# Performance work log

Hardware: AMD Instinct MI355X
Metric: run time of the kernel (lower is better)

## Reference

```python
import jax, jax.numpy as jnp
import numpy as np

VSN = 1e-12  # VERY_SMALL_NUMBER
B, N, IN_DIM = 48, 512, 400
ENC, HID, OUT, NREL = 256, 128, 128, 53
NUM_PERS, KNN, EPS, SKIP = 4, 10, 0.3, 0.8


def setup_inputs() -> dict:
    key = jax.random.key(0)
    ks = jax.random.split(key, 12)
    context = jax.random.normal(ks[0], (B, N, IN_DIM), dtype=jnp.float32)
    context_lens = jax.random.randint(ks[1], (B,), N // 2, N + 1)
    s1 = jax.random.randint(ks[2], (B,), 0, N - 16)
    e1 = s1 + jax.random.randint(ks[3], (B,), 1, 8)
    s2 = jax.random.randint(ks[4], (B,), 0, N - 16)
    e2 = s2 + jax.random.randint(ks[5], (B,), 1, 8)
    mentions = jnp.stack([s1, e1, s2, e2], axis=-1)  # [B,4]
    sc = lambda d: 1.0 / np.sqrt(d)
    w_enc = jax.random.normal(ks[6], (IN_DIM, ENC), dtype=jnp.float32) * sc(IN_DIM)
    b_enc = jnp.zeros((ENC,), jnp.float32)
    gl_weight = jax.random.normal(ks[7], (NUM_PERS, IN_DIM), dtype=jnp.float32)
    gcn_w1 = jax.random.normal(ks[8], (ENC, HID), dtype=jnp.float32) * sc(ENC)
    gcn_b1 = jnp.zeros((HID,), jnp.float32)
    gcn_w2 = jax.random.normal(ks[9], (HID, OUT), dtype=jnp.float32) * sc(HID)
    gcn_b2 = jnp.zeros((OUT,), jnp.float32)
    lin_w = jax.random.normal(ks[10], (OUT, NREL), dtype=jnp.float32) * sc(OUT)
    lin_b = jnp.zeros((NREL,), jnp.float32)
    return dict(context=context, context_lens=context_lens, mentions=mentions,
                w_enc=w_enc, b_enc=b_enc, gl_weight=gl_weight,
                gcn_w1=gcn_w1, gcn_b1=gcn_b1, gcn_w2=gcn_w2, gcn_b2=gcn_b2,
                lin_w=lin_w, lin_b=lin_b)


def _knn_init_adj(feats, mask):
    # binarized kNN graph on raw features + symmetric normalization
    mask2d = mask[:, :, None] * mask[:, None, :]
    att = jnp.einsum('bnd,bmd->bnm', feats, feats) * mask2d
    _, idx = jax.lax.top_k(att, KNN)                      # [B,N,K]
    adj = jnp.zeros((B, N, N), feats.dtype).at[
        jnp.arange(B)[:, None, None], jnp.arange(N)[None, :, None], idx].set(1.0)
    adj = adj * mask2d
    rowsum = jnp.clip(adj.sum(-1), VSN, None)
    rinv = (rowsum ** -0.5) * mask                        # [B,N]
    return rinv[:, :, None] * adj * rinv[:, None, :]


def _weighted_cosine(feats, gl_weight, mask):
    # multi-perspective weighted cosine similarity, epsilon-sparsified (>=0 adj)
    ctx = feats[None] * gl_weight[:, None, None, :]       # [P,B,N,D]
    ctx = ctx / jnp.clip(jnp.linalg.norm(ctx, axis=-1, keepdims=True), VSN, None)
    att = jnp.einsum('pbnd,pbmd->pbnm', ctx, ctx).mean(0)  # [B,N,N]
    mask2d = mask[:, :, None] * mask[:, None, :]
    att = att * mask2d                                    # markoff_value = 0
    return att * (att > EPS).astype(att.dtype)


def _merge(enc_seq, start, end):
    w_ids = jnp.arange(N)[None, :]                        # [1,N]
    ind = ((w_ids >= start[:, None]) & (w_ids <= end[:, None])).astype(enc_seq.dtype)
    return jnp.einsum('bn,bnd->bd', ind, enc_seq) / ind.sum(-1, keepdims=True)


def reference(context, context_lens, mentions, w_enc, b_enc, gl_weight,
              gcn_w1, gcn_b1, gcn_w2, gcn_b2, lin_w, lin_b):
    mask = (jnp.arange(N)[None, :] < context_lens[:, None]).astype(jnp.float32)
    # init kNN adjacency on detached raw features
    init_adj = _knn_init_adj(jax.lax.stop_gradient(context), mask)
    # context encoder (linear projection stand-in for the LSTM ctx_encoder)
    enc = context @ w_enc + b_enc                          # [B,N,ENC]
    # learned graph: row-normalize then skip-connect with init_adj
    raw_adj = _weighted_cosine(context, gl_weight, mask)
    adj = raw_adj / jnp.clip(raw_adj.sum(-1, keepdims=True), VSN, None)
    adj = SKIP * init_adj + (1.0 - SKIP) * adj
    # 2-hop GCN encoder
    h = jax.nn.relu(jnp.einsum('bnm,bmd->bnd', adj, enc) @ gcn_w1 + gcn_b1)
    node_vec = jnp.einsum('bnm,bmd->bnd', adj, h) @ gcn_w2 + gcn_b2  # [B,N,OUT]
    # graph maxpool over nodes + mention merging (broadcast-mask averaging)
    pooled = node_vec.max(axis=1)                          # [B,OUT]
    arg1 = _merge(node_vec, mentions[:, 0], mentions[:, 1])
    arg2 = _merge(node_vec, mentions[:, 2], mentions[:, 3])
    return (pooled + arg1 + arg2) @ lin_w + lin_b          # [B,NREL]
```

## Files before the change

kernel.cpp:

```cpp
#include <hip/hip_runtime.h>
#include <math.h>

constexpr int cB = 48, cN = 512, cIN = 400;
constexpr int cENC = 256, cHID = 128, cOUT = 128, cNREL = 53;
constexpr int cKNN = 10;
constexpr float cVSN = 1e-12f;
constexpr float cEPS = 0.3f;

constexpr int KP = 416;
constexpr size_t ARRSZ = (size_t)cB * cN * KP;
constexpr int NBN = cB * cN;
constexpr size_t NADJ = (size_t)cB * cN * cN;
constexpr size_t NE1 = (size_t)NBN * 128;

typedef _Float16 f16;
typedef _Float16 f16x8 __attribute__((ext_vector_type(8)));
typedef float f32x4 __attribute__((ext_vector_type(4)));

__device__ inline void gload16(const void* g, void* l) {
    __builtin_amdgcn_global_load_lds(
        (const __attribute__((address_space(1))) unsigned int*)g,
        (__attribute__((address_space(3))) unsigned int*)l, 16, 0, 0);
}

#define MFMA16(a, b, c) __builtin_amdgcn_mfma_f32_16x16x32_f16((a), (b), (c), 0, 0, 0)

__global__ __launch_bounds__(256) void k_prep0(
    const float* __restrict__ X,
    const float* __restrict__ w_enc, const float* __restrict__ w1,
    const float* __restrict__ b_enc, const float* __restrict__ w2,
    f16* __restrict__ XH, f16* __restrict__ XL,
    f16* __restrict__ wc1H, float* __restrict__ bc1p, f16* __restrict__ w2tH)
{
    int bid = blockIdx.x;
    int t = threadIdx.x;
    if (bid <= KP) {
        int d = bid;
        __shared__ float wred[2][128];
        int o = t & 127, half = t >> 7;
        if (d < cIN) {
            float acc = 0.f;
            const float* we = w_enc + (size_t)d * cENC + half * 128;
            const float* w1p = w1 + (size_t)half * 128 * cHID + o;
            #pragma unroll 8
            for (int e = 0; e < 128; ++e) acc += we[e] * w1p[(size_t)e * cHID];
            wred[half][o] = acc;
            __syncthreads();
            if (half == 0) wc1H[(size_t)o * KP + d] = (f16)(wred[0][o] + wred[1][o]);
        } else if (d < KP) {
            if (t < 128) wc1H[(size_t)o * KP + d] = (f16)0.f;
        } else {
            float acc = 0.f;
            const float* w1p = w1 + (size_t)half * 128 * cHID + o;
            #pragma unroll 8
            for (int e = 0; e < 128; ++e) acc += b_enc[half * 128 + e] * w1p[(size_t)e * cHID];
            wred[half][o] = acc;
            __syncthreads();
            if (half == 0) bc1p[o] = wred[0][o] + wred[1][o];
        }
        if (d < cHID && t < 128) w2tH[(size_t)t * cHID + d] = (f16)w2[(size_t)d * cOUT + t];
        return;
    }
    int row = (bid - (KP + 1)) * 4 + (t >> 6);
    int k8 = t & 63;
    if (k8 >= 52) return;
    size_t obase = (size_t)row * KP + k8 * 8;
    if (k8 < 50) {
        const float* x = X + (size_t)row * cIN + k8 * 8;
        float4 xa = *(const float4*)x;
        float4 xb = *(const float4*)(x + 4);
        float xv[8] = {xa.x, xa.y, xa.z, xa.w, xb.x, xb.y, xb.z, xb.w};
        f16x8 vh, vl;
        #pragma unroll
        for (int e = 0; e < 8; ++e) {
            f16 hh = (f16)xv[e];
            vh[e] = hh;
            vl[e] = (f16)(xv[e] - (float)hh);
        }
        *(f16x8*)(XH + obase) = vh;
        *(f16x8*)(XL + obase) = vl;
    } else {
        f16x8 z = (f16x8)(f16)0.f;
        *(f16x8*)(XH + obase) = z;
        *(f16x8*)(XL + obase) = z;
    }
}

__global__ __launch_bounds__(256) void k_norms(const float* __restrict__ X,
                                               const int* __restrict__ lens,
                                               const float* __restrict__ glw,
                                               float* __restrict__ maskA,
                                               float* __restrict__ invnM)
{
    int row = blockIdx.x;
    int t = threadIdx.x;
    int w = t >> 6, lane = t & 63;
    __shared__ float sw[4];
    int b = row >> 9, n = row & (cN - 1);
    float s = 0.f;
    if (lane < 50) {
        int k = lane * 8;
        const float* x = X + (size_t)row * cIN + k;
        const float* g = glw + (size_t)w * cIN + k;
        float4 xa = *(const float4*)x, xb = *(const float4*)(x + 4);
        float4 ga = *(const float4*)g, gb = *(const float4*)(g + 4);
        float xv[8] = {xa.x, xa.y, xa.z, xa.w, xb.x, xb.y, xb.z, xb.w};
        float gv[8] = {ga.x, ga.y, ga.z, ga.w, gb.x, gb.y, gb.z, gb.w};
        #pragma unroll
        for (int e = 0; e < 8; ++e) {
            float tt = xv[e] * gv[e];
            s += tt * tt;
        }
    }
    #pragma unroll
    for (int off = 32; off; off >>= 1) s += __shfl_xor(s, off, 64);
    if (lane == 0) sw[w] = s;
    __syncthreads();
    if (t == 0) {
        float m = (n < lens[b]) ? 1.0f : 0.0f;
        float4 iv;
        iv.x = m / fmaxf(sqrtf(sw[0]), cVSN);
        iv.y = m / fmaxf(sqrtf(sw[1]), cVSN);
        iv.z = m / fmaxf(sqrtf(sw[2]), cVSN);
        iv.w = m / fmaxf(sqrtf(sw[3]), cVSN);
        *(float4*)&invnM[(size_t)row * 4] = iv;
        maskA[row] = m;
    }
}

__global__ __launch_bounds__(256, 3) void k_sim_mfma(
    const f16* __restrict__ XH, const f16* __restrict__ XL,
    const float* __restrict__ glw, const int* __restrict__ lens,
    const float* __restrict__ maskA, const float* __restrict__ invnM,
    float* __restrict__ G0, f16* __restrict__ RAh)
{
    int L = blockIdx.x + (blockIdx.y << 3) + (blockIdx.z << 6);
    int xcd = L & 7, j0 = L >> 3;
    int work = xcd * 384 + j0;
    const int b = work >> 6;
    int rem = work & 63;
    const int n0 = (rem >> 3) * 64, m0 = (rem & 7) * 64;

    const int t = threadIdx.x;
    const int w = t >> 6, lane = t & 63;
    const int wr = w >> 1, wc = w & 1;
    const int lr = lane & 15, lc = lane >> 4;

    const size_t rowBaseB = (size_t)b * cN;
    const int len = lens[b];

    if (n0 >= len || m0 >= len) return;

    __shared__ f16 lds[3][8192];
    __shared__ f16 w2l[4][KP];

    for (int i = t; i < 4 * KP; i += 256) {
        int p = i / KP, d = i - p * KP;
        float g = (d < cIN) ? glw[p * cIN + d] : 0.f;
        w2l[p][d] = (f16)(g * g);
    }

    f32x4 accG[2][2], accP[4][2][2];
    #pragma unroll
    for (int i = 0; i < 2; ++i)
        #pragma unroll
        for (int jj = 0; jj < 2; ++jj) {
            accG[i][jj] = (f32x4)0.f;
            #pragma unroll
            for (int p = 0; p < 4; ++p) accP[p][i][jj] = (f32x4)0.f;
        }

    constexpr int NPAN = KP / 32;

#define SIM_STAGE(buf, pan) do { \
    const int kk0_ = (pan) * 32; \
    _Pragma("unroll") \
    for (int q = 0; q < 4; ++q) { \
        int c_ = w + q * 4;                \
        int tt_ = c_ >> 2, rq_ = c_ & 3; \
        int row_ = rq_ * 16 + (lane >> 2); \
        int kcg_ = (lane & 3) ^ (row_ & 3) ^ ((row_ >> 2) & 3); \
        const f16* arr_ = (tt_ & 1) ? XL : XH; \
        int rb_ = (tt_ < 2) ? n0 : m0; \
        const f16* g_ = arr_ + (rowBaseB + rb_ + row_) * (size_t)KP + kk0_ + kcg_ * 8; \
        gload16(g_, (void*)&lds[buf][tt_ * 2048 + rq_ * 512]); \
    } \
} while (0)

    SIM_STAGE(0, 0);
    SIM_STAGE(1, 1);
    __syncthreads();

    for (int pan = 0; pan < NPAN; ++pan) {
        int cur = pan % 3;
        if (pan + 2 < NPAN) SIM_STAGE((pan + 2) % 3, pan + 2);
        const f16x8* L8 = (const f16x8*)lds[cur];
        const int kk0 = pan * 32;
        f16x8 aH[2], aL[2], bH[2], bL[2], wp[4];
        #pragma unroll
        for (int i = 0; i < 2; ++i) {
            int r = wr * 32 + i * 16 + lr;
            int cell = r * 4 + (lc ^ (r & 3) ^ ((r >> 2) & 3));
            aH[i] = L8[cell];
            aL[i] = L8[256 + cell];
        }
        #pragma unroll
        for (int jj = 0; jj < 2; ++jj) {
            int r = wc * 32 + jj * 16 + lr;
            int cell = r * 4 + (lc ^ (r & 3) ^ ((r >> 2) & 3));
            bH[jj] = L8[512 + cell];
            bL[jj] = L8[768 + cell];
        }
        #pragma unroll
        for (int p = 0; p < 4; ++p) wp[p] = *(const f16x8*)&w2l[p][kk0 + lc * 8];

        __builtin_amdgcn_s_setprio(1);
        #pragma unroll
        for (int i = 0; i < 2; ++i)
            #pragma unroll
            for (int jj = 0; jj < 2; ++jj) {
                accG[i][jj] = MFMA16(aH[i], bH[jj], accG[i][jj]);
                accG[i][jj] = MFMA16(aH[i], bL[jj], accG[i][jj]);
                accG[i][jj] = MFMA16(aL[i], bH[jj], accG[i][jj]);
            }
        #pragma unroll
        for (int p = 0; p < 4; ++p)
            #pragma unroll
            for (int i = 0; i < 2; ++i) {
                f16x8 ap = aH[i] * wp[p];
                #pragma unroll
                for (int jj = 0; jj < 2; ++jj)
                    accP[p][i][jj] = MFMA16(ap, bH[jj], accP[p][i][jj]);
            }
        __builtin_amdgcn_s_setprio(0);

        if (pan < NPAN - 1) {
            if (pan + 2 < NPAN) {
                asm volatile("s_waitcnt vmcnt(4)" ::: "memory");
            } else {
                asm volatile("s_waitcnt vmcnt(0)" ::: "memory");
            }
            asm volatile("s_waitcnt lgkmcnt(0)" ::: "memory");
            __builtin_amdgcn_s_barrier();
        }
    }
#undef SIM_STAGE

    #pragma unroll
    for (int i = 0; i < 2; ++i) {
        #pragma unroll
        for (int jj = 0; jj < 2; ++jj) {
            int m = m0 + wc * 32 + jj * 16 + lr;
            size_t rowm = rowBaseB + m;
            float mskm = maskA[rowm];
            float4 im = *(const float4*)&invnM[rowm * 4];
            #pragma unroll
            for (int v = 0; v < 4; ++v) {
                int n = n0 + wr * 32 + i * 16 + lc * 4 + v;
                size_t rown = rowBaseB + n;
                float4 in_ = *(const float4*)&invnM[rown * 4];
                float g = accG[i][jj][v] * maskA[rown] * mskm;
                float s = 0.25f * (accP[0][i][jj][v] * in_.x * im.x
                                 + accP[1][i][jj][v] * in_.y * im.y
                                 + accP[2][i][jj][v] * in_.z * im.z
                                 + accP[3][i][jj][v] * in_.w * im.w);
                float rv = (s > cEPS) ? s : 0.f;
                __builtin_nontemporal_store(g, &G0[rown * cN + m]);
                RAh[rown * cN + m] = (f16)rv;
            }
        }
    }
}

__global__ void k_topk(const float* __restrict__ G0, const float* __restrict__ mask,
                       const int* __restrict__ lens,
                       int* __restrict__ kidx, float* __restrict__ rinv)
{
    int row = blockIdx.x * 4 + (threadIdx.x >> 6);
    int lane = threadIdx.x & 63;
    int b = row >> 9, n = row & (cN - 1);
    int len = lens[b];
    if (n >= len) {
        if (lane < cKNN) kidx[row * cKNN + lane] = lane;
        if (lane == 0) rinv[row] = 0.f;
        return;
    }
    int lenc = (len + 63) & ~63;
    const float* g = G0 + (long long)row * cN;
    float val[8];
    #pragma unroll
    for (int k = 0; k < 8; ++k) {
        int col = lane + 64 * k;
        val[k] = (col < lenc) ? __builtin_nontemporal_load(&g[col]) : -INFINITY;
    }
    float cnt = 0.f;
    long long mbase = (long long)b * cN;
    for (int r = 0; r < cKNN; ++r) {
        float best = val[0];
        #pragma unroll
        for (int k = 1; k < 8; ++k) best = fmaxf(best, val[k]);
        #pragma unroll
        for (int off = 32; off; off >>= 1) best = fmaxf(best, __shfl_xor(best, off, 64));
        int sl = -1;
        #pragma unroll
        for (int k = 7; k >= 0; --k) if (val[k] == best) sl = k;
        unsigned long long holders = __ballot(sl >= 0);
        int src = (int)(__ffsll((long long)holders) - 1);
        int mycol = lane + (sl << 6);
        int col = __shfl(mycol, src, 64);
        if (lane == src) val[sl] = -INFINITY;
        if (lane == 0) {
            kidx[row * cKNN + r] = col;
            cnt += mask[mbase + col];
        }
    }
    if (lane == 0) rinv[row] = rsqrtf(fmaxf(cnt, cVSN));
}

__global__ void k_adj2(const f16* __restrict__ RAh, const float* __restrict__ rinv,
                       const int* __restrict__ kidx, const int* __restrict__ lens,
                       f16* __restrict__ adjH, float* __restrict__ adjrs)
{
    int row = blockIdx.x;
    int t = threadIdx.x;
    int b = row >> 9, n = row & (cN - 1);
    int len = lens[b];
    long long base = (long long)row * cN;
    if (n >= len) {
        adjH[base + t] = (f16)0.f;
        adjH[base + t + 256] = (f16)0.f;
        if (t == 0) adjrs[row] = 0.f;
        return;
    }
    int w = t >> 6, lane = t & 63;
    __shared__ int sidx[cKNN];
    __shared__ float srv[cKNN];
    __shared__ float red[4];
    long long bbase = (long long)(row & ~(cN - 1));
    if (t < cKNN) {
        int c = kidx[row * cKNN + t];
        sidx[t] = c;
        srv[t] = rinv[bbase + c];
    }
    float ra0 = (t < len) ? (float)RAh[base + t] : 0.f;
    float ra1 = (t + 256 < len) ? (float)RAh[base + t + 256] : 0.f;
    float s = ra0 + ra1;
    #pragma unroll
    for (int off = 32; off; off >>= 1) s += __shfl_xor(s, off, 64);
    if (lane == 0) red[w] = s;
    __syncthreads();
    float rsum = red[0] + red[1] + red[2] + red[3];
    float inv_rs = 1.0f / fmaxf(rsum, cVSN);
    float rn = rinv[row];
    float osum = 0.f;
    #pragma unroll
    for (int mi = 0; mi < 2; ++mi) {
        int m = t + mi * 256;
        float ra = mi ? ra1 : ra0;
        float v = 0.2f * ra * inv_rs;
        #pragma unroll
        for (int k = 0; k < cKNN; ++k)
            if (m == sidx[k]) v += 0.8f * rn * srv[k];
        adjH[base + m] = (f16)v;
        osum += v;
    }
    #pragma unroll
    for (int off = 32; off; off >>= 1) osum += __shfl_xor(osum, off, 64);
    __syncthreads();
    if (lane == 0) red[w] = osum;
    __syncthreads();
    if (t == 0) adjrs[row] = red[0] + red[1] + red[2] + red[3];
}

template<int BIAS, bool RELU, int OMODE, bool ADJA>
__global__ __launch_bounds__(256, 4) void k_gemm1(
    const f16* __restrict__ A, const f16* __restrict__ Bp,
    long long bStrideB, int K, const int* __restrict__ lens,
    const float* __restrict__ biasv, const float* __restrict__ bc1p,
    const float* __restrict__ adjrs, const int* __restrict__ ments,
    f16* __restrict__ CH, float* __restrict__ part)
{
    int L = blockIdx.x + blockIdx.y * gridDim.x;
    int work = (L & 7) * 96 + (L >> 3);
    const int R0 = (work >> 1) * 64;
    const int bn0 = (work & 1) * 64;
    const int bidx = R0 >> 9;
    const int t = threadIdx.x, w = t >> 6, lane = t & 63;
    const int wr = w >> 1, wc = w & 1, lr = lane & 15, lc = lane >> 4;
    __shared__ f16 lds[3][4096];
    __shared__ float sred[2][3][64];
    const f16* Bb = Bp + (size_t)bidx * bStrideB + (size_t)bn0 * K;

    f32x4 acc[2][2];
    #pragma unroll
    for (int i = 0; i < 2; ++i)
        #pragma unroll
        for (int jj = 0; jj < 2; ++jj) acc[i][jj] = (f32x4)0.f;

#define G1_STAGE(buf, p_) do { \
    const int k0_ = (p_) * 32; \
    _Pragma("unroll") \
    for (int q = 0; q < 2; ++q) { \
        int c_ = w + q * 4; \
        int rq_ = c_ & 3; \
        int row_ = rq_ * 16 + (lane >> 2); \
        int kc_ = (lane & 3) ^ (row_ & 3) ^ ((row_ >> 2) & 3); \
        const f16* src_ = (c_ < 4) ? (A + (size_t)(R0 + row_) * K + k0_ + kc_ * 8) \
                                   : (Bb + (size_t)row_ * K + k0_ + kc_ * 8); \
        gload16(src_, (void*)&lds[buf][(c_ >> 2) * 2048 + rq_ * 512]); \
    } \
} while (0)

    int npan = K >> 5;
    bool skipA = false;
    if (ADJA) {
        int lenb = lens[bidx];
        npan = (lenb + 31) >> 5;
        skipA = ((R0 & (cN - 1)) >= lenb);
    }
    if (!skipA) {
        G1_STAGE(0, 0);
        G1_STAGE(1, 1);
        __syncthreads();
        for (int p = 0; p < npan; ++p) {
            int cur = p % 3;
            if (p + 2 < npan) G1_STAGE((p + 2) % 3, p + 2);
            const f16x8* L8 = (const f16x8*)lds[cur];
            f16x8 af[2], bf[2];
            #pragma unroll
            for (int i = 0; i < 2; ++i) {
                int r = wr * 32 + i * 16 + lr;
                int cell = r * 4 + (lc ^ (r & 3) ^ ((r >> 2) & 3));
                af[i] = L8[cell];
            }
            #pragma unroll
            for (int jj = 0; jj < 2; ++jj) {
                int r = wc * 32 + jj * 16 + lr;
                int cell = r * 4 + (lc ^ (r & 3) ^ ((r >> 2) & 3));
                bf[jj] = L8[256 + cell];
            }
            __builtin_amdgcn_s_setprio(1);
            #pragma unroll
            for (int i = 0; i < 2; ++i)
                #pragma unroll
                for (int jj = 0; jj < 2; ++jj)
                    acc[i][jj] = MFMA16(af[i], bf[jj], acc[i][jj]);
            __builtin_amdgcn_s_setprio(0);
            if (p < npan - 1) {
                if (p + 2 < npan) {
                    asm volatile("s_waitcnt vmcnt(2)" ::: "memory");
                } else {
                    asm volatile("s_waitcnt vmcnt(0)" ::: "memory");
                }
                asm volatile("s_waitcnt lgkmcnt(0)" ::: "memory");
                __builtin_amdgcn_s_barrier();
            }
        }
    }
#undef G1_STAGE

    if (OMODE != 2) {
        #pragma unroll
        for (int i = 0; i < 2; ++i)
            #pragma unroll
            for (int jj = 0; jj < 2; ++jj) {
                int col = bn0 + wc * 32 + jj * 16 + lr;
                #pragma unroll
                for (int v = 0; v < 4; ++v) {
                    int r = R0 + wr * 32 + i * 16 + lc * 4 + v;
                    float val = acc[i][jj][v];
                    if (BIAS == 2) val += adjrs[r] * bc1p[col] + biasv[col];
                    if (RELU) val = fmaxf(val, 0.f);
                    size_t addr = (OMODE == 1)
                        ? ((size_t)(r >> 9) * 65536 + (size_t)col * 512 + (r & 511))
                        : ((size_t)r * 128 + col);
                    CH[addr] = (f16)val;
                }
            }
    } else {
        const int b = bidx, rb = (R0 >> 6) & 7, cb = bn0 >> 6;
        int s1 = ments[b * 4 + 0], e1 = ments[b * 4 + 1];
        int s2 = ments[b * 4 + 2], e2 = ments[b * 4 + 3];
        #pragma unroll
        for (int jj = 0; jj < 2; ++jj) {
            int col = bn0 + wc * 32 + jj * 16 + lr;
            float vmax = -INFINITY, v1 = 0.f, v2 = 0.f;
            #pragma unroll
            for (int i = 0; i < 2; ++i)
                #pragma unroll
                for (int v = 0; v < 4; ++v) {
                    int gn = (R0 & 511) + wr * 32 + i * 16 + lc * 4 + v;
                    float val = acc[i][jj][v] + biasv[col];
                    vmax = fmaxf(vmax, val);
                    if (gn >= s1 && gn <= e1) v1 += val;
                    if (gn >= s2 && gn <= e2) v2 += val;
                }
            #pragma unroll
            for (int off = 16; off <= 32; off <<= 1) {
                vmax = fmaxf(vmax, __shfl_xor(vmax, off, 64));
                v1 += __shfl_xor(v1, off, 64);
                v2 += __shfl_xor(v2, off, 64);
            }
            if (lc == 0) {
                int c = wc * 32 + jj * 16 + lr;
                sred[wr][0][c] = vmax;
                sred[wr][1][c] = v1;
                sred[wr][2][c] = v2;
            }
        }
        __syncthreads();
        if (t < 192) {
            int m = t >> 6, c = t & 63;
            float a0 = sred[0][m][c], a1v = sred[1][m][c];
            float comb = (m == 0) ? fmaxf(a0, a1v) : (a0 + a1v);
            part[((((size_t)b * 8 + rb) * 2 + cb) * 3 + m) * 64 + c] = comb;
        }
    }
}

__global__ void k_final2(const float* __restrict__ part, const int* __restrict__ mentions,
                         const float* __restrict__ lw, const float* __restrict__ lb,
                         float* __restrict__ out)
{
    int b = blockIdx.x;
    int t = threadIdx.x;
    __shared__ float vec[128];
    int s1 = mentions[b * 4 + 0], e1 = mentions[b * 4 + 1];
    int s2 = mentions[b * 4 + 2], e2 = mentions[b * 4 + 3];
    int cb = t >> 6, c = t & 63;
    float pm = -INFINITY, s1s = 0.f, s2s = 0.f;
    #pragma unroll
    for (int rb = 0; rb < 8; ++rb) {
        size_t base = ((((size_t)b * 8 + rb) * 2 + cb) * 3) * 64 + c;
        pm = fmaxf(pm, part[base]);
        s1s += part[base + 64];
        s2s += part[base + 128];
    }
    vec[t] = pm + s1s / (float)(e1 - s1 + 1) + s2s / (float)(e2 - s2 + 1);
    __syncthreads();
    if (t < cNREL) {
        float s = lb[t];
        for (int dd = 0; dd < cOUT; ++dd) s += vec[dd] * lw[dd * cNREL + t];
        out[b * cNREL + t] = s;
    }
}

extern "C" void kernel_launch(void* const* d_in, const int* in_sizes, int n_in,
                              void* d_out, int out_size, void* d_ws, size_t ws_size,
                              hipStream_t stream)
{
    const float* context = (const float*)d_in[0];
    const int*   lens    = (const int*)d_in[1];
    const int*   ments   = (const int*)d_in[2];
    const float* w_enc   = (const float*)d_in[3];
    const float* b_enc   = (const float*)d_in[4];
    const float* glw     = (const float*)d_in[5];
    const float* w1      = (const float*)d_in[6];
    const float* b1      = (const float*)d_in[7];
    const float* w2      = (const float*)d_in[8];
    const float* b2      = (const float*)d_in[9];
    const float* lw      = (const float*)d_in[10];
    const float* lb      = (const float*)d_in[11];
    float* out = (float*)d_out;

    f16* XH   = (f16*)d_ws;
    f16* XL   = XH + ARRSZ;
    f16* adjH = XL + ARRSZ;
    f16* E1t  = adjH + NADJ;
    f16* hH   = E1t + NE1;
    f16* H2t  = hH + NE1;
    f16* RAh  = H2t + NE1;
    float* G0 = (float*)(RAh + NADJ);
    float* invnM = G0 + NADJ;
    float* maskA = invnM + 4 * NBN;
    float* rinv  = maskA + NBN;
    float* adjrs = rinv + NBN;
    float* part  = adjrs + NBN;
    float* bc1p  = part + 147456;
    f16* wc1H = (f16*)(bc1p + 128);
    f16* w2tH = wc1H + (size_t)128 * KP;
    int* kidx = (int*)(w2tH + 128 * 128);

    k_prep0<<<KP + 1 + NBN / 4, 256, 0, stream>>>(
        context, w_enc, w1, b_enc, w2, XH, XL, wc1H, bc1p, w2tH);
    k_norms<<<NBN, 256, 0, stream>>>(context, lens, glw, maskA, invnM);
    k_sim_mfma<<<dim3(8, 8, cB), 256, 0, stream>>>(XH, XL, glw, lens, maskA, invnM, G0, RAh);
    k_topk<<<NBN / 4, 256, 0, stream>>>(G0, maskA, lens, kidx, rinv);
    k_adj2<<<NBN, 256, 0, stream>>>(RAh, rinv, kidx, lens, adjH, adjrs);

    k_gemm1<0, false, 1, false><<<dim3(NBN / 64, 2), 256, 0, stream>>>(
        XH, wc1H, 0, KP, nullptr, nullptr, nullptr, nullptr, nullptr, E1t, nullptr);
    k_gemm1<2, true, 0, true><<<dim3(NBN / 64, 2), 256, 0, stream>>>(
        adjH, E1t, 65536, cN, lens, b1, bc1p, adjrs, nullptr, hH, nullptr);
    k_gemm1<0, false, 1, false><<<dim3(NBN / 64, 2), 256, 0, stream>>>(
        hH, w2tH, 0, cHID, nullptr, nullptr, nullptr, nullptr, nullptr, H2t, nullptr);
    k_gemm1<0, false, 2, true><<<dim3(NBN / 64, 2), 256, 0, stream>>>(
        adjH, H2t, 65536, cN, lens, b2, nullptr, nullptr, ments, nullptr, part);

    k_final2<<<cB, 128, 0, stream>>>(part, ments, lw, lb, out);
}
```

Baseline: 200.9 us.

## Exploit similarity symmetry: compute upper-triangle tiles and mirror via LDS transpose

```diff
diff --git a/kernel.cpp b/kernel.cpp
--- a/kernel.cpp
+++ b/kernel.cpp
@@ -149,7 +149,7 @@
     const size_t rowBaseB = (size_t)b * cN;
     const int len = lens[b];
 
-    if (n0 >= len || m0 >= len) return;
+    if (n0 >= len || m0 >= len || n0 > m0) return;
 
     __shared__ f16 lds[3][8192];
     __shared__ f16 w2l[4][KP];
@@ -246,18 +246,24 @@
     }
 #undef SIM_STAGE
 
+    __syncthreads();
+    float* sG = (float*)lds;
+    f16*   sR = (f16*)((float*)lds + 64 * 65);
+    const bool offdiag = (n0 != m0);
+
     #pragma unroll
     for (int i = 0; i < 2; ++i) {
         #pragma unroll
         for (int jj = 0; jj < 2; ++jj) {
-            int m = m0 + wc * 32 + jj * 16 + lr;
+            int ml = wc * 32 + jj * 16 + lr;
+            int m = m0 + ml;
             size_t rowm = rowBaseB + m;
             float mskm = maskA[rowm];
             float4 im = *(const float4*)&invnM[rowm * 4];
             #pragma unroll
             for (int v = 0; v < 4; ++v) {
-                int n = n0 + wr * 32 + i * 16 + lc * 4 + v;
-                size_t rown = rowBaseB + n;
+                int nl = wr * 32 + i * 16 + lc * 4 + v;
+                size_t rown = rowBaseB + n0 + nl;
                 float4 in_ = *(const float4*)&invnM[rown * 4];
                 float g = accG[i][jj][v] * maskA[rown] * mskm;
                 float s = 0.25f * (accP[0][i][jj][v] * in_.x * im.x
@@ -267,7 +273,24 @@
                 float rv = (s > cEPS) ? s : 0.f;
                 __builtin_nontemporal_store(g, &G0[rown * cN + m]);
                 RAh[rown * cN + m] = (f16)rv;
-            }
+                if (offdiag) {
+                    sG[nl * 65 + ml] = g;
+                    sR[nl * 66 + ml] = (f16)rv;
+                }
+            }
+        }
+    }
+    if (offdiag) {
+        __syncthreads();
+        #pragma unroll
+        for (int e = 0; e < 16; ++e) {
+            int idx = t + e * 256;
+            int mr = idx >> 6, nc = idx & 63;
+            size_t rowm = rowBaseB + m0 + mr;
+            float gv = sG[nc * 65 + mr];
+            f16 rvv = sR[nc * 66 + mr];
+            __builtin_nontemporal_store(gv, &G0[rowm * cN + n0 + nc]);
+            RAh[rowm * cN + n0 + nc] = rvv;
         }
     }
 }
```

New measurement: 184.2 us. 1.09x faster.
